# Kernel tuning notes

Measured on AMD Instinct MI355X. Metric: run time of the kernel, lower is better.

Reference implementation:

```python
import jax, jax.numpy as jnp
import numpy as np

B, T, C, H = 8, 1024, 1024, 8
D = C // H  # head dim

def setup_inputs() -> dict:
    key = jax.random.key(0)
    ks = jax.random.split(key, 6)
    s = 1.0 / np.sqrt(C)
    return {
        "x": jax.random.normal(ks[0], (B, T, C), jnp.float32),
        "mask": jnp.ones((B, T), jnp.int32),
        "Wq": jax.random.normal(ks[1], (C, C), jnp.float32) * s,
        "bq": jnp.zeros((C,), jnp.float32),
        "Wk": jax.random.normal(ks[2], (C, C), jnp.float32) * s,
        "bk": jnp.zeros((C,), jnp.float32),
        "Wv": jax.random.normal(ks[3], (C, C), jnp.float32) * s,
        "bv": jnp.zeros((C,), jnp.float32),
        "Wp": jax.random.normal(ks[4], (C, C), jnp.float32) * s,
        "bp": jnp.zeros((C,), jnp.float32),
    }

def reference(x, mask, Wq, bq, Wk, bk, Wv, bv, Wp, bp):
    # torch Linear: x @ W.T + b
    q = (x @ Wq.T + bq).reshape(B, T, H, D).transpose(0, 2, 1, 3)  # b h t d
    k = (x @ Wk.T + bk).reshape(B, T, H, D).transpose(0, 2, 1, 3)
    v = (x @ Wv.T + bv).reshape(B, T, H, D).transpose(0, 2, 1, 3)
    att = jnp.einsum('bhqd,bhkd->bhqk', q, k) * (1.0 / np.sqrt(D))
    m = mask.astype(jnp.float32)[:, None, None, :]  # (B,1,1,T)
    att = jnp.where(m == 0, -jnp.inf, att)
    att = jax.nn.softmax(att, axis=-1)
    y = jnp.einsum('bhqk,bhkd->bhqd', att, v)
    y = y.transpose(0, 2, 1, 3).reshape(B, T, C)
    return y @ Wp.T + bp
```

## Files before the change

kernel.cpp:

```cpp
#include <hip/hip_runtime.h>

typedef __bf16 bf16;
typedef __attribute__((ext_vector_type(8))) bf16 bf16x8;
typedef __attribute__((ext_vector_type(4))) float f32x4;

#define GLDS16(g, l) __builtin_amdgcn_global_load_lds( \
    (const __attribute__((address_space(1))) void*)(g), \
    (__attribute__((address_space(3))) void*)(l), 16, 0, 0)

#define QSCALE 0.12751744f

static __device__ __forceinline__ f32x4 MFMA(bf16x8 a, bf16x8 b, f32x4 c) {
    return __builtin_amdgcn_mfma_f32_16x16x32_bf16(a, b, c, 0, 0, 0);
}

__global__ __launch_bounds__(256) void convert_kernel(
    const float* __restrict__ x, const float* __restrict__ wq,
    const float* __restrict__ wk, const float* __restrict__ wv,
    const float* __restrict__ wp,
    bf16* __restrict__ xb, bf16* __restrict__ wqkvb, bf16* __restrict__ wpb)
{
    int bid = blockIdx.x;
    const float* src; bf16* dst; int base;
    if (bid < 4096)      { src = x;  dst = xb;              base = bid * 2048; }
    else if (bid < 4608) { src = wq; dst = wqkvb;           base = (bid - 4096) * 2048; }
    else if (bid < 5120) { src = wk; dst = wqkvb + 1048576; base = (bid - 4608) * 2048; }
    else if (bid < 5632) { src = wv; dst = wqkvb + 2097152; base = (bid - 5120) * 2048; }
    else                 { src = wp; dst = wpb;             base = (bid - 5632) * 2048; }
    int i = base + threadIdx.x * 8;
    const f32x4* s4 = (const f32x4*)(src + i);
    f32x4 a = s4[0], c = s4[1];
    bf16x8 v;
    #pragma unroll
    for (int e = 0; e < 4; ++e) { v[e] = (bf16)a[e]; v[e + 4] = (bf16)c[e]; }
    *(bf16x8*)(dst + i) = v;
}

template <int MODE, int NTN>
__global__ __launch_bounds__(256, 2) void gemm2(
    const bf16* __restrict__ A, const bf16* __restrict__ B,
    const float* __restrict__ bias0, const float* __restrict__ bias1,
    const float* __restrict__ bias2,
    bf16* __restrict__ q_out, bf16* __restrict__ k_out, bf16* __restrict__ vt_out,
    float* __restrict__ f_out)
{
    constexpr int K = 1024;
    constexpr int NT = K / 64;
    constexpr int NWG = 64 * NTN;
    const int tid = threadIdx.x;
    const int lane = tid & 63;
    const int wid = tid >> 6;
    const int wr = wid >> 1, wc = wid & 1;
    const int l15 = lane & 15, l4 = lane >> 4, l7 = lane & 7;

    const int g = blockIdx.x;
    const int lin = (g & 7) * (NWG / 8) + (g >> 3);
    const int m0 = (lin / NTN) * 128, n0 = (lin % NTN) * 128;

    __shared__ __align__(16) bf16 lds[2][2][8192];

    const int rr = tid >> 3, pc = tid & 7;
    auto stage = [&](int buf, int t) {
        #pragma unroll
        for (int c = 0; c < 4; ++c) {
            int row = c * 32 + rr;
            int lc = pc ^ (row & 7);
            GLDS16(A + (size_t)(m0 + row) * K + t * 64 + lc * 8,
                   &lds[buf][0][c * 2048 + tid * 8]);
        }
        #pragma unroll
        for (int c = 0; c < 4; ++c) {
            int row = c * 32 + rr;
            int lc = pc ^ (row & 7);
            GLDS16(B + (size_t)(n0 + row) * K + t * 64 + lc * 8,
                   &lds[buf][1][c * 2048 + tid * 8]);
        }
    };

    const int arow = wr * 64 + l15;
    const int brow = wc * 64 + l15;
    #define RA(buf, f, kk) (*(const bf16x8*)((const char*)lds[buf][0] + \
        (arow + (f) * 16) * 128 + ((((kk) * 4 + l4) ^ l7) * 16)))
    #define RB(buf, j, kk) (*(const bf16x8*)((const char*)lds[buf][1] + \
        (brow + (j) * 16) * 128 + ((((kk) * 4 + l4) ^ l7) * 16)))

    f32x4 acc[4][4];
    #pragma unroll
    for (int f = 0; f < 4; ++f)
        #pragma unroll
        for (int j = 0; j < 4; ++j)
            #pragma unroll
            for (int e = 0; e < 4; ++e) acc[f][j][e] = 0.f;

    stage(0, 0);
    __syncthreads();

    for (int t = 0; t < NT; ++t) {
        const int buf = t & 1;
        if (t + 1 < NT) stage(buf ^ 1, t + 1);
        bf16x8 af[4][2], bfr[4][2];
        #pragma unroll
        for (int f = 0; f < 4; ++f) { af[f][0] = RA(buf, f, 0); af[f][1] = RA(buf, f, 1); }
        #pragma unroll
        for (int j = 0; j < 4; ++j) { bfr[j][0] = RB(buf, j, 0); bfr[j][1] = RB(buf, j, 1); }
        __builtin_amdgcn_s_setprio(1);
        #pragma unroll
        for (int f = 0; f < 4; ++f)
            #pragma unroll
            for (int j = 0; j < 4; ++j) {
                acc[f][j] = MFMA(af[f][0], bfr[j][0], acc[f][j]);
                acc[f][j] = MFMA(af[f][1], bfr[j][1], acc[f][j]);
            }
        __builtin_amdgcn_s_setprio(0);
        __syncthreads();
    }
    #undef RA
    #undef RB

    #pragma unroll
    for (int f = 0; f < 4; ++f) {
        #pragma unroll
        for (int j = 0; j < 4; ++j) {
            #pragma unroll
            for (int r = 0; r < 4; ++r) {
                int m = m0 + wr * 64 + f * 16 + l4 * 4 + r;
                int n = n0 + wc * 64 + j * 16 + l15;
                float v = acc[f][j][r];
                if (MODE == 0) {
                    if (n0 < 1024) {
                        q_out[m * 1024 + n] = (bf16)((v + bias0[n]) * QSCALE);
                    } else if (n0 < 2048) {
                        int nn = n - 1024;
                        k_out[m * 1024 + nn] = (bf16)(v + bias1[nn]);
                    } else {
                        int nn = n - 2048;
                        int hl = nn >> 7, d = nn & 127;
                        int bb = m >> 10, tt = m & 1023;
                        vt_out[((bb * 8 + hl) * 128 + d) * 1024 + tt] = (bf16)(v + bias2[nn]);
                    }
                } else {
                    f_out[m * 1024 + n] = v + bias0[n];
                }
            }
        }
    }
}

__global__ __launch_bounds__(256, 2) void attn_kernel(
    const bf16* __restrict__ qb, const bf16* __restrict__ kb,
    const bf16* __restrict__ vtb, const int* __restrict__ mask,
    bf16* __restrict__ yb)
{
    const int tid = threadIdx.x;
    const int lane = tid & 63;
    const int wid = tid >> 6;
    const int g = blockIdx.x;
    const int orig = (g & 7) * 128 + (g >> 3);
    const int bh = orig >> 4;
    const int qt = orig & 15;
    const int b = bh >> 3;
    const int h = bh & 7;
    const int m0 = b * 1024 + qt * 64;

    __shared__ __align__(16) char smem[73728];

    auto stageKV = [&](int bufKV, int kt) {
        char* Kb = smem + bufKV * 16384;
        char* Vb = smem + 32768 + bufKV * 16384;
        #pragma unroll
        for (int n = 0; n < 4; ++n)
            GLDS16(kb + (b * 1024 + kt + n * 16 + (tid >> 4)) * 1024 + h * 128 +
                       (((tid & 15) ^ ((tid >> 4) & 7)) * 8),
                   Kb + n * 4096 + tid * 16);
        #pragma unroll
        for (int n = 0; n < 4; ++n)
            GLDS16(vtb + (bh * 128 + n * 32 + (tid >> 3)) * 1024 + kt +
                       (((tid & 7) ^ ((tid >> 3) & 7)) * 8),
                   Vb + n * 4096 + tid * 16);
    };

    bf16x8 qf[4];
    #pragma unroll
    for (int kc = 0; kc < 4; ++kc)
        qf[kc] = *(const bf16x8*)(qb + (m0 + wid * 16 + (lane & 15)) * 1024 +
                                  h * 128 + kc * 32 + (lane >> 4) * 8);

    f32x4 o[8];
    #pragma unroll
    for (int jd = 0; jd < 8; ++jd)
        #pragma unroll
        for (int e = 0; e < 4; ++e) o[jd][e] = 0.f;
    float l_run[4] = {0.f, 0.f, 0.f, 0.f};

    stageKV(0, 0);
    __syncthreads();

    for (int t = 0; t < 16; ++t) {
        const int buf = t & 1;
        const int kt = t * 64;
        if (t + 1 < 16) stageKV(buf ^ 1, kt + 64);

        int mv[4];
        #pragma unroll
        for (int j = 0; j < 4; ++j)
            mv[j] = mask[b * 1024 + kt + j * 16 + (lane & 15)];

        const char* Ks = smem + buf * 16384;
        const char* Vs = smem + 32768 + buf * 16384;

        f32x4 s[4];
        #pragma unroll
        for (int j = 0; j < 4; ++j)
            #pragma unroll
            for (int e = 0; e < 4; ++e) s[j][e] = 0.f;
        #pragma unroll
        for (int kc = 0; kc < 4; ++kc) {
            bf16x8 kf[4];
            #pragma unroll
            for (int j = 0; j < 4; ++j)
                kf[j] = *(const bf16x8*)(Ks +
                    (j * 16 + (lane & 15)) * 256 +
                    (((kc * 4 + (lane >> 4)) ^ (lane & 7)) * 16));
            #pragma unroll
            for (int j = 0; j < 4; ++j)
                s[j] = __builtin_amdgcn_mfma_f32_16x16x32_bf16(qf[kc], kf[j], s[j], 0, 0, 0);
        }

        #pragma unroll
        for (int j = 0; j < 4; ++j) {
            if (mv[j] == 0) {
                #pragma unroll
                for (int e = 0; e < 4; ++e) s[j][e] = -1e30f;
            }
            #pragma unroll
            for (int r = 0; r < 4; ++r) {
                float p = __builtin_amdgcn_exp2f(s[j][r]);
                s[j][r] = p;
                l_run[r] += p;
            }
        }

        #pragma unroll
        for (int j = 0; j < 4; ++j)
            #pragma unroll
            for (int r = 0; r < 4; ++r) {
                int row = (lane >> 4) * 4 + r;
                int col = j * 16 + (lane & 15);
                *(bf16*)(smem + 65536 + wid * 2048 + row * 128 +
                         (((col >> 3) ^ (row & 7)) * 16) + (col & 7) * 2) = (bf16)s[j][r];
            }

        #pragma unroll
        for (int k2 = 0; k2 < 2; ++k2) {
            bf16x8 pa = *(const bf16x8*)(smem + 65536 + wid * 2048 +
                (lane & 15) * 128 + (((k2 * 4 + (lane >> 4)) ^ (lane & 7)) * 16));
            #pragma unroll
            for (int jd = 0; jd < 8; ++jd) {
                bf16x8 vf = *(const bf16x8*)(Vs +
                    (jd * 16 + (lane & 15)) * 128 +
                    (((k2 * 4 + (lane >> 4)) ^ (lane & 7)) * 16));
                o[jd] = __builtin_amdgcn_mfma_f32_16x16x32_bf16(pa, vf, o[jd], 0, 0, 0);
            }
        }
        __syncthreads();
    }

    #pragma unroll
    for (int off = 8; off >= 1; off >>= 1)
        #pragma unroll
        for (int r = 0; r < 4; ++r) l_run[r] += __shfl_xor(l_run[r], off);
    float inv[4];
    #pragma unroll
    for (int r = 0; r < 4; ++r) inv[r] = 1.0f / fmaxf(l_run[r], 1e-30f);
    #pragma unroll
    for (int jd = 0; jd < 8; ++jd)
        #pragma unroll
        for (int r = 0; r < 4; ++r)
            yb[(m0 + wid * 16 + (lane >> 4) * 4 + r) * 1024 +
               h * 128 + jd * 16 + (lane & 15)] = (bf16)(o[jd][r] * inv[r]);
}

extern "C" void kernel_launch(void* const* d_in, const int* in_sizes, int n_in,
                              void* d_out, int out_size, void* d_ws, size_t ws_size,
                              hipStream_t stream)
{
    (void)in_sizes; (void)n_in; (void)out_size; (void)ws_size;
    const float* x  = (const float*)d_in[0];
    const int* mask = (const int*)d_in[1];
    const float* Wq = (const float*)d_in[2];
    const float* bq = (const float*)d_in[3];
    const float* Wk = (const float*)d_in[4];
    const float* bk = (const float*)d_in[5];
    const float* Wv = (const float*)d_in[6];
    const float* bv = (const float*)d_in[7];
    const float* Wp = (const float*)d_in[8];
    const float* bp = (const float*)d_in[9];
    float* out = (float*)d_out;

    char* ws = (char*)d_ws;
    bf16* xb    = (bf16*)(ws);
    bf16* wqkvb = (bf16*)(ws + (16u << 20));
    bf16* wpb   = (bf16*)(ws + (22u << 20));
    bf16* qbuf  = (bf16*)(ws + (24u << 20));
    bf16* kbuf  = (bf16*)(ws + (40u << 20));
    bf16* vtb   = (bf16*)(ws + (56u << 20));
    bf16* ybuf  = (bf16*)(ws + (72u << 20));

    convert_kernel<<<6144, 256, 0, stream>>>(x, Wq, Wk, Wv, Wp, xb, wqkvb, wpb);
    gemm2<0, 24><<<1536, 256, 0, stream>>>(xb, wqkvb, bq, bk, bv,
                                           qbuf, kbuf, vtb, nullptr);
    attn_kernel<<<1024, 256, 0, stream>>>(qbuf, kbuf, vtb, mask, ybuf);
    gemm2<1, 8><<<512, 256, 0, stream>>>(ybuf, wpb, bp, nullptr, nullptr,
                                         nullptr, nullptr, nullptr, out);
}
```

Baseline: 185.5 us.

## Halve GEMM K-tile to 32 with new swizzled LDS layout for higher occupancy

Shrinks the GEMM K-step from 64 to 32, halving LDS per block (32KB to 16KB) and fragment registers. Launch bounds go to 4 blocks per SM, and the LDS layout now packs two rows per 128-byte line with an XOR swizzle. The aim is more resident waves to hide global-to-LDS latency. In exchange the K loop has twice as many iterations and barriers, with less MFMA work per sync.

```diff
diff --git a/kernel.cpp b/kernel.cpp
--- a/kernel.cpp
+++ b/kernel.cpp
@@ -37,7 +37,7 @@
 }
 
 template <int MODE, int NTN>
-__global__ __launch_bounds__(256, 2) void gemm2(
+__global__ __launch_bounds__(256, 4) void gemm2(
     const bf16* __restrict__ A, const bf16* __restrict__ B,
     const float* __restrict__ bias0, const float* __restrict__ bias1,
     const float* __restrict__ bias2,
@@ -45,44 +45,47 @@
     float* __restrict__ f_out)
 {
     constexpr int K = 1024;
-    constexpr int NT = K / 64;
+    constexpr int NT = K / 32;
     constexpr int NWG = 64 * NTN;
     const int tid = threadIdx.x;
     const int lane = tid & 63;
     const int wid = tid >> 6;
     const int wr = wid >> 1, wc = wid & 1;
-    const int l15 = lane & 15, l4 = lane >> 4, l7 = lane & 7;
+    const int l15 = lane & 15, l4 = lane >> 4;
 
     const int g = blockIdx.x;
     const int lin = (g & 7) * (NWG / 8) + (g >> 3);
     const int m0 = (lin / NTN) * 128, n0 = (lin % NTN) * 128;
 
-    __shared__ __align__(16) bf16 lds[2][2][8192];
-
-    const int rr = tid >> 3, pc = tid & 7;
+    __shared__ __align__(16) bf16 lds[2][2][4096];
+
+    const int ln0 = tid >> 3, pc = tid & 7;
     auto stage = [&](int buf, int t) {
         #pragma unroll
-        for (int c = 0; c < 4; ++c) {
-            int row = c * 32 + rr;
-            int lc = pc ^ (row & 7);
-            GLDS16(A + (size_t)(m0 + row) * K + t * 64 + lc * 8,
-                   &lds[buf][0][c * 2048 + tid * 8]);
-        }
-        #pragma unroll
-        for (int c = 0; c < 4; ++c) {
-            int row = c * 32 + rr;
-            int lc = pc ^ (row & 7);
-            GLDS16(B + (size_t)(n0 + row) * K + t * 64 + lc * 8,
-                   &lds[buf][1][c * 2048 + tid * 8]);
+        for (int half = 0; half < 2; ++half) {
+            int line = half * 32 + ln0;
+            int q = pc ^ (line & 7);
+            int row = 2 * line + (q >> 2);
+            int c = q & 3;
+            GLDS16(A + (size_t)(m0 + row) * K + t * 32 + c * 8,
+                   &lds[buf][0][half * 2048 + tid * 8]);
+        }
+        #pragma unroll
+        for (int half = 0; half < 2; ++half) {
+            int line = half * 32 + ln0;
+            int q = pc ^ (line & 7);
+            int row = 2 * line + (q >> 2);
+            int c = q & 3;
+            GLDS16(B + (size_t)(n0 + row) * K + t * 32 + c * 8,
+                   &lds[buf][1][half * 2048 + tid * 8]);
         }
     };
 
-    const int arow = wr * 64 + l15;
-    const int brow = wc * 64 + l15;
-    #define RA(buf, f, kk) (*(const bf16x8*)((const char*)lds[buf][0] + \
-        (arow + (f) * 16) * 128 + ((((kk) * 4 + l4) ^ l7) * 16)))
-    #define RB(buf, j, kk) (*(const bf16x8*)((const char*)lds[buf][1] + \
-        (brow + (j) * 16) * 128 + ((((kk) * 4 + l4) ^ l7) * 16)))
+    const int physc = (((l15 & 1) * 4 + l4) ^ ((l15 >> 1) & 7)) * 16;
+    const int aoff = (wr * 32 + (l15 >> 1)) * 128 + physc;
+    const int boff = (wc * 32 + (l15 >> 1)) * 128 + physc;
+    #define RA(buf, f) (*(const bf16x8*)((const char*)lds[buf][0] + aoff + (f) * 1024))
+    #define RB(buf, j) (*(const bf16x8*)((const char*)lds[buf][1] + boff + (j) * 1024))
 
     f32x4 acc[4][4];
     #pragma unroll
@@ -98,19 +101,17 @@
     for (int t = 0; t < NT; ++t) {
         const int buf = t & 1;
         if (t + 1 < NT) stage(buf ^ 1, t + 1);
-        bf16x8 af[4][2], bfr[4][2];
-        #pragma unroll
-        for (int f = 0; f < 4; ++f) { af[f][0] = RA(buf, f, 0); af[f][1] = RA(buf, f, 1); }
-        #pragma unroll
-        for (int j = 0; j < 4; ++j) { bfr[j][0] = RB(buf, j, 0); bfr[j][1] = RB(buf, j, 1); }
+        bf16x8 af[4], bfr[4];
+        #pragma unroll
+        for (int f = 0; f < 4; ++f) af[f] = RA(buf, f);
+        #pragma unroll
+        for (int j = 0; j < 4; ++j) bfr[j] = RB(buf, j);
         __builtin_amdgcn_s_setprio(1);
         #pragma unroll
         for (int f = 0; f < 4; ++f)
             #pragma unroll
-            for (int j = 0; j < 4; ++j) {
-                acc[f][j] = MFMA(af[f][0], bfr[j][0], acc[f][j]);
-                acc[f][j] = MFMA(af[f][1], bfr[j][1], acc[f][j]);
-            }
+            for (int j = 0; j < 4; ++j)
+                acc[f][j] = MFMA(af[f], bfr[j], acc[f][j]);
         __builtin_amdgcn_s_setprio(0);
         __syncthreads();
     }
@@ -163,7 +164,6 @@
     const int m0 = b * 1024 + qt * 64;
 
     __shared__ __align__(16) char smem[73728];
-
     auto stageKV = [&](int bufKV, int kt) {
         char* Kb = smem + bufKV * 16384;
         char* Vb = smem + 32768 + bufKV * 16384;
```

New measurement: 182.4 us. Within noise of the previous version (-1.7%).
